# Optimization experiments

Measured on AMD Instinct MI355X. Metric: run time of the kernel, lower is better.

The kernel has to match this reference:

```python
import jax, jax.numpy as jnp
import numpy as np

GRID_SIZE = 5
SPLINE_ORDER = 3
GRID_LO, GRID_HI = -1.0, 1.0
K = 3  # kernel height/width


def setup_inputs() -> dict:
    key = jax.random.key(0)
    k1, k2, k3 = jax.random.split(key, 3)
    x = jax.random.uniform(k1, (32, 256, 256), dtype=jnp.float32)
    base_weight = jax.random.normal(k2, (K, K), dtype=jnp.float32)
    spline_weight = jax.random.normal(k3, (K, K, GRID_SIZE + SPLINE_ORDER), dtype=jnp.float32)
    return {"x": x, "base_weight": base_weight, "spline_weight": spline_weight}


def _b_splines(xe, grid):
    # xe: (..., 1); grid: (G + 2s + 1,) -> bases (..., G + s)
    bases = ((xe >= grid[:-1]) & (xe < grid[1:])).astype(xe.dtype)
    for k in range(1, SPLINE_ORDER + 1):
        left = (xe - grid[: -(k + 1)]) / (grid[k:-1] - grid[: -(k + 1)])
        right = (grid[k + 1:] - xe) / (grid[k + 1:] - grid[1:-k])
        bases = left * bases[..., :-1] + right * bases[..., 1:]
    return bases


def reference(x, base_weight, spline_weight):
    h = (GRID_HI - GRID_LO) / GRID_SIZE
    # grid buffer: arange(-s, G+s+1)*h + lo, identical across kernel positions
    grid = jnp.arange(-SPLINE_ORDER, GRID_SIZE + SPLINE_ORDER + 1, dtype=x.dtype) * h + GRID_LO
    B, H, W = x.shape
    Ho, Wo = H - K + 1, W - K + 1
    # sliding-window patches, stride 1, no padding: (B, Ho, Wo, K*K)
    patches = jnp.stack(
        [x[:, a:a + Ho, b:b + Wo] for a in range(K) for b in range(K)], axis=-1
    )
    bases = _b_splines(patches[..., None], grid)  # (B, Ho, Wo, K*K, G+s)
    sw = spline_weight.reshape(K * K, GRID_SIZE + SPLINE_ORDER)
    spline_out = jnp.einsum('bhwpc,pc->bhw', bases, sw)
    base_out = jnp.einsum('bhwp,p->bhw', jax.nn.silu(patches), base_weight.reshape(-1))
    return spline_out + base_out
```

## Files before the change

### kernel.cpp

```cpp
#include <hip/hip_runtime.h>
#include <math.h>

#define H_IN   256
#define W_IN   256
#define BATCH  32
#define Ho     254
#define Wo     254
#define TROWS  16


__global__ __launch_bounds__(256, 2)
void kan_conv_kernel(const float* __restrict__ x,
                     const float* __restrict__ bw,
                     const float* __restrict__ sw,
                     float* __restrict__ out)
{
    const int w     = threadIdx.x;
    const int strip = blockIdx.x;
    const int b     = blockIdx.y;
    if (w >= Wo) return;

    float W_base[9];
    float W_sp[9][6];
#pragma unroll
    for (int p = 0; p < 9; ++p) {
        W_base[p] = bw[p];
#pragma unroll
        for (int m = 0; m < 6; ++m) W_sp[p][m] = sw[p * 8 + 2 + m];
    }

    const int h0   = strip * TROWS;
    const int hEnd = min(h0 + TROWS, Ho);

    const float* xb = x   + (size_t)b * (H_IN * W_IN);
    float*       ob = out + (size_t)b * (Ho * Wo);

    float qq0 = 0.f, q0p = 0.f, q1p = 0.f;

    for (int r = h0; r < hEnd + 2; ++r) {
        float f[3][7];
#pragma unroll
        for (int c = 0; c < 3; ++c) {
            const float xv = xb[r * W_IN + w + c];

            const float sg = __fdividef(xv, 1.f + __expf(-xv));

            const float t  = (xv + 2.2f) * 2.5f;
            const float fj = floorf(t);
            const float u  = t - fj;

            const float u2 = u * u;
            const float u3 = u2 * u;
            const float om = 1.f - u;
            const float B0 = om * om * om * (1.f / 6.f);
            const float B1 = (3.f * u3 - 6.f * u2 + 4.f) * (1.f / 6.f);
            const float B2 = (-3.f * u3 + 3.f * u2 + 3.f * u + 1.f) * (1.f / 6.f);
            const float B3 = u3 * (1.f / 6.f);

            const bool r0 = (fj == 5.f);
            const bool r1 = (fj == 6.f);
            const bool r2 = (fj == 7.f);

            f[c][0] = sg;
            f[c][1] = r0 ? B0 : 0.f;
            f[c][2] = r0 ? B1 : (r1 ? B0 : 0.f);
            f[c][3] = r0 ? B2 : (r1 ? B1 : B0);
            f[c][4] = r0 ? B3 : (r1 ? B2 : B1);
            f[c][5] = r1 ? B3 : (r2 ? B2 : 0.f);
            f[c][6] = r2 ? B3 : 0.f;
        }

        float q0 = 0.f, q1 = 0.f, q2 = 0.f;
#pragma unroll
        for (int a = 0; a < 3; ++a) {
            float acc = 0.f;
#pragma unroll
            for (int c = 0; c < 3; ++c) {
                const int p = a * 3 + c;
                float s = f[c][0] * W_base[p];
#pragma unroll
                for (int m = 0; m < 6; ++m) s += f[c][1 + m] * W_sp[p][m];
                acc += s;
            }
            if (a == 0) q0 = acc;
            else if (a == 1) q1 = acc;
            else q2 = acc;
        }

        if (r >= h0 + 2) {
            const int h = r - 2;
            ob[h * Wo + w] = qq0 + q1p + q2;
        }
        qq0 = q0p;
        q0p = q0;
        q1p = q1;
    }
}

extern "C" void kernel_launch(void* const* d_in, const int* in_sizes, int n_in,
                              void* d_out, int out_size, void* d_ws, size_t ws_size,
                              hipStream_t stream) {
    const float* x  = (const float*)d_in[0];
    const float* bw = (const float*)d_in[1];
    const float* sw = (const float*)d_in[2];
    float* out = (float*)d_out;

    dim3 grid((Ho + TROWS - 1) / TROWS, BATCH);
    dim3 block(256);
    kan_conv_kernel<<<grid, block, 0, stream>>>(x, bw, sw, out);
}
```

Measured before the change: 77.73 us.

## Prefetch next input row, shrink row strips, and simplify spline basis math

Each thread now loads the next row's three inputs while computing the current row, so global-load latency overlaps with arithmetic. The row strip height drops from 16 to 8 and the launch-bounds occupancy hint rises from 2 to 4 blocks, giving more blocks and waves at the cost of more halo rows recomputed per strip. The spline setup uses a fused multiply-add for the knot position, and the basis evaluation derives B2 from the partition of unity and B1 with an FMA. The accumulation is written as explicit FMA chains into the three row sums. The occupancy hint may force register pressure, and computing B2 by subtraction changes rounding slightly.

```diff
diff --git a/kernel.cpp b/kernel.cpp
--- a/kernel.cpp
+++ b/kernel.cpp
@@ -6,46 +6,55 @@
 #define BATCH  32
 #define Ho     254
 #define Wo     254
-#define TROWS  16
+#define TROWS  8
 
 
-__global__ __launch_bounds__(256, 2)
+__global__ __launch_bounds__(256, 4)
 void kan_conv_kernel(const float* __restrict__ x,
                      const float* __restrict__ bw,
                      const float* __restrict__ sw,
                      float* __restrict__ out)
 {
-    const int w     = threadIdx.x;
+    const int w = threadIdx.x;
+    if (w >= Wo) return;
     const int strip = blockIdx.x;
     const int b     = blockIdx.y;
-    if (w >= Wo) return;
 
-    float W_base[9];
-    float W_sp[9][6];
+    float W7[9][7];
 #pragma unroll
     for (int p = 0; p < 9; ++p) {
-        W_base[p] = bw[p];
+        W7[p][0] = bw[p];
 #pragma unroll
-        for (int m = 0; m < 6; ++m) W_sp[p][m] = sw[p * 8 + 2 + m];
+        for (int m = 0; m < 6; ++m) W7[p][1 + m] = sw[p * 8 + 2 + m];
     }
 
     const int h0   = strip * TROWS;
     const int hEnd = min(h0 + TROWS, Ho);
 
     const float* xb = x   + (size_t)b * (H_IN * W_IN);
-    float*       ob = out + (size_t)b * (Ho * Wo);
+    float*       ob = out + (size_t)b * (Ho * Wo) + w;
+
+    float cx0 = xb[h0 * W_IN + w];
+    float cx1 = xb[h0 * W_IN + w + 1];
+    float cx2 = xb[h0 * W_IN + w + 2];
 
     float qq0 = 0.f, q0p = 0.f, q1p = 0.f;
 
-    for (int r = h0; r < hEnd + 2; ++r) {
-        float f[3][7];
+    for (int r = h0; r <= hEnd + 1; ++r) {
+        const int rn = (r <= hEnd) ? r + 1 : r;
+        const float* np = xb + rn * W_IN + w;
+        const float nx0 = np[0];
+        const float nx1 = np[1];
+        const float nx2 = np[2];
+
+        float q0 = 0.f, q1 = 0.f, q2 = 0.f;
 #pragma unroll
         for (int c = 0; c < 3; ++c) {
-            const float xv = xb[r * W_IN + w + c];
+            const float xv = (c == 0) ? cx0 : (c == 1) ? cx1 : cx2;
 
             const float sg = __fdividef(xv, 1.f + __expf(-xv));
 
-            const float t  = (xv + 2.2f) * 2.5f;
+            const float t  = __fmaf_rn(xv, 2.5f, 5.5f);
             const float fj = floorf(t);
             const float u  = t - fj;
 
@@ -53,47 +62,45 @@
             const float u3 = u2 * u;
             const float om = 1.f - u;
             const float B0 = om * om * om * (1.f / 6.f);
-            const float B1 = (3.f * u3 - 6.f * u2 + 4.f) * (1.f / 6.f);
-            const float B2 = (-3.f * u3 + 3.f * u2 + 3.f * u + 1.f) * (1.f / 6.f);
             const float B3 = u3 * (1.f / 6.f);
+            const float B1 = __fmaf_rn(0.5f, u3, (2.f / 3.f) - u2);
+            const float B2 = 1.f - B0 - B1 - B3;
 
             const bool r0 = (fj == 5.f);
             const bool r1 = (fj == 6.f);
             const bool r2 = (fj == 7.f);
 
-            f[c][0] = sg;
-            f[c][1] = r0 ? B0 : 0.f;
-            f[c][2] = r0 ? B1 : (r1 ? B0 : 0.f);
-            f[c][3] = r0 ? B2 : (r1 ? B1 : B0);
-            f[c][4] = r0 ? B3 : (r1 ? B2 : B1);
-            f[c][5] = r1 ? B3 : (r2 ? B2 : 0.f);
-            f[c][6] = r2 ? B3 : 0.f;
-        }
+            const float f0 = sg;
+            const float f1 = r0 ? B0 : 0.f;
+            const float f2 = r0 ? B1 : (r1 ? B0 : 0.f);
+            const float f3 = r0 ? B2 : (r1 ? B1 : B0);
+            const float f4 = r0 ? B3 : (r1 ? B2 : B1);
+            const float f5 = r1 ? B3 : (r2 ? B2 : 0.f);
+            const float f6 = r2 ? B3 : 0.f;
 
-        float q0 = 0.f, q1 = 0.f, q2 = 0.f;
 #pragma unroll
-        for (int a = 0; a < 3; ++a) {
-            float acc = 0.f;
-#pragma unroll
-            for (int c = 0; c < 3; ++c) {
-                const int p = a * 3 + c;
-                float s = f[c][0] * W_base[p];
-#pragma unroll
-                for (int m = 0; m < 6; ++m) s += f[c][1 + m] * W_sp[p][m];
-                acc += s;
+            for (int a = 0; a < 3; ++a) {
+                const float* Wp = W7[a * 3 + c];
+                float acc = (a == 0) ? q0 : (a == 1) ? q1 : q2;
+                acc = __fmaf_rn(f0, Wp[0], acc);
+                acc = __fmaf_rn(f1, Wp[1], acc);
+                acc = __fmaf_rn(f2, Wp[2], acc);
+                acc = __fmaf_rn(f3, Wp[3], acc);
+                acc = __fmaf_rn(f4, Wp[4], acc);
+                acc = __fmaf_rn(f5, Wp[5], acc);
+                acc = __fmaf_rn(f6, Wp[6], acc);
+                if (a == 0) q0 = acc; else if (a == 1) q1 = acc; else q2 = acc;
             }
-            if (a == 0) q0 = acc;
-            else if (a == 1) q1 = acc;
-            else q2 = acc;
         }
 
         if (r >= h0 + 2) {
-            const int h = r - 2;
-            ob[h * Wo + w] = qq0 + q1p + q2;
+            ob[(r - 2) * Wo] = qq0 + q1p + q2;
         }
         qq0 = q0p;
         q0p = q0;
         q1p = q1;
+
+        cx0 = nx0; cx1 = nx1; cx2 = nx2;
     }
 }
 
```

Result: faster. 73.22 us (-5.8%).
